# Performance work log

Hardware: AMD Instinct MI355X
Metric: run time of the kernel (lower is better)

## Reference

```python
import jax, jax.numpy as jnp
import numpy as np

SCALE = 100.0
ACTIVE_EPS = 1e-6


def setup_inputs() -> dict:
    key = jax.random.key(0)
    kq, kk, kv = jax.random.split(key, 3)
    B, K, D = 64, 1024, 512
    return {
        "query": jax.random.normal(kq, (B, D), dtype=jnp.float32),
        "keys": jax.random.normal(kk, (K, D), dtype=jnp.float32),
        "values": jax.random.normal(kv, (K, D), dtype=jnp.float32),
    }


def _scores(query, keys):
    # Fused, batched version of the per-key PureFFN score layers.
    # Layer k has W_up = diag(S * key[k] * d^-0.5) on active dims (|key|>1e-6),
    # b_gate = 1 on active dims, W_down[0] = 1/S on active dims. The extra
    # hidden unit (row `dim`) has zero W_down weight and never contributes.
    # PureFFN: out = W_down @ (h * sigmoid(h + b_gate)), h = W_up @ x.
    D = query.shape[-1]
    scale = D ** -0.5
    active = (jnp.abs(keys) > ACTIVE_EPS).astype(query.dtype)      # [K, D]
    u = (SCALE * scale) * query[:, None, :] * keys[None, :, :]     # [B, K, D]
    g = u * jax.nn.sigmoid(u + active[None, :, :])                 # silu with b_gate=1 on active dims
    return (1.0 / SCALE) * jnp.einsum('bkd,kd->bk', g, active)    # [B, K]


def reference(query, keys, values):
    scores = _scores(query, keys)            # [B, K]
    winner_idx = jnp.argmax(scores, axis=-1)  # [B] int
    out_values = values[winner_idx]           # [B, D] winner-take-all gather
    return out_values, winner_idx
```

## Files before the change

kernel.cpp:

```cpp
#include <hip/hip_runtime.h>
#include <stdint.h>

#define NB 64
#define NK 1024
#define ND 512
#define ROWS 2
#define CHUNKS 64
#define KEYS_PER_BLOCK (NK / CHUNKS)
#define WAVES_PER_BLOCK 4
#define KEYS_PER_WAVE (KEYS_PER_BLOCK / WAVES_PER_BLOCK)

typedef float v2f __attribute__((ext_vector_type(2)));

#if __has_builtin(__builtin_amdgcn_exp2f)
#define EXP2F(x) __builtin_amdgcn_exp2f(x)
#else
#define EXP2F(x) exp2f(x)
#endif
#if __has_builtin(__builtin_amdgcn_rcpf)
#define RCPF(x) __builtin_amdgcn_rcpf(x)
#else
#define RCPF(x) (1.0f / (x))
#endif

__device__ __forceinline__ void silu2_acc(v2f qc, v2f kv, v2f& acc) {
    const float NL2E = -1.4426950408889634f;
    v2f u = qc * kv;
    v2f y = u * NL2E + NL2E;
    v2f e;
    e.x = EXP2F(y.x);
    e.y = EXP2F(y.y);
    v2f f = e + 1.0f;
    float r = RCPF(f.x * f.y);
    v2f sg;
    sg.x = r * f.y;
    sg.y = r * f.x;
    acc += u * sg;
}

__device__ __forceinline__ unsigned long long pack_win(float s, int k) {
    uint32_t bits = __float_as_uint(s);
    uint32_t so = (bits & 0x80000000u) ? ~bits : (bits | 0x80000000u);
    return ((unsigned long long)so << 32) | (unsigned long long)(uint32_t)(NK - 1 - k);
}

__global__ __launch_bounds__(256, 8) void sia_scores(const float* __restrict__ q,
                                                     const float* __restrict__ keys,
                                                     unsigned long long* __restrict__ ws) {
    const int bidx = blockIdx.x;
    const int bg    = bidx >> 6;
    const int chunk = bidx & (CHUNKS - 1);
    const int tid = threadIdx.x;
    const int wave = tid >> 6;
    const int lane = tid & 63;

    const float C = 100.0f * 0.04419417382415922f;

    v2f qv[ROWS][4];
    #pragma unroll
    for (int r = 0; r < ROWS; ++r) {
        const v2f* q2 = reinterpret_cast<const v2f*>(q + (bg * ROWS + r) * ND + lane * 8);
        #pragma unroll
        for (int j = 0; j < 4; ++j)
            qv[r][j] = q2[j] * C;
    }

    const int k0 = chunk * KEYS_PER_BLOCK + wave * KEYS_PER_WAVE;

    v2f acc[ROWS][KEYS_PER_WAVE];
    #pragma unroll
    for (int r = 0; r < ROWS; ++r)
        #pragma unroll
        for (int i = 0; i < KEYS_PER_WAVE; ++i)
            acc[r][i] = (v2f)0.0f;

    #pragma unroll
    for (int i = 0; i < KEYS_PER_WAVE; ++i) {
        const float4* k4 = reinterpret_cast<const float4*>(keys + (k0 + i) * ND + lane * 8);
        float4 ka = k4[0];
        float4 kb = k4[1];
        v2f kv[4];
        kv[0] = (v2f){ka.x, ka.y};
        kv[1] = (v2f){ka.z, ka.w};
        kv[2] = (v2f){kb.x, kb.y};
        kv[3] = (v2f){kb.z, kb.w};
        #pragma unroll
        for (int r = 0; r < ROWS; ++r)
            #pragma unroll
            for (int j = 0; j < 4; ++j)
                silu2_acc(qv[r][j], kv[j], acc[r][i]);
    }

    float sc[ROWS][KEYS_PER_WAVE];
    #pragma unroll
    for (int r = 0; r < ROWS; ++r)
        #pragma unroll
        for (int i = 0; i < KEYS_PER_WAVE; ++i)
            sc[r][i] = acc[r][i].x + acc[r][i].y;

    #pragma unroll
    for (int off = 32; off > 0; off >>= 1) {
        #pragma unroll
        for (int r = 0; r < ROWS; ++r)
            #pragma unroll
            for (int i = 0; i < KEYS_PER_WAVE; ++i)
                sc[r][i] += __shfl_xor(sc[r][i], off, 64);
    }

    __shared__ unsigned long long win[WAVES_PER_BLOCK][ROWS];
    if (lane == 0) {
        #pragma unroll
        for (int r = 0; r < ROWS; ++r) {
            float best_s = sc[r][0];
            int best_j = 0;
            #pragma unroll
            for (int i = 1; i < KEYS_PER_WAVE; ++i)
                if (sc[r][i] > best_s) { best_s = sc[r][i]; best_j = i; }
            win[wave][r] = pack_win(best_s, k0 + best_j);
        }
    }
    __syncthreads();

    if (tid < ROWS) {
        const int r = tid;
        unsigned long long p = win[0][r];
        #pragma unroll
        for (int w = 1; w < WAVES_PER_BLOCK; ++w)
            if (win[w][r] > p) p = win[w][r];
        ws[(bg * ROWS + r) * CHUNKS + chunk] = p;
    }
}

__global__ __launch_bounds__(128) void sia_final(const unsigned long long* __restrict__ ws,
                                                 const float* __restrict__ values,
                                                 float* __restrict__ out) {
    const int b = blockIdx.x;
    const int tid = threadIdx.x;
    const int lane = tid & 63;

    unsigned long long p = ws[b * CHUNKS + lane];
    #pragma unroll
    for (int off = 32; off > 0; off >>= 1) {
        unsigned long long o = __shfl_xor(p, off, 64);
        if (o > p) p = o;
    }
    const int k = NK - 1 - (int)((uint32_t)p & 0x3FFu);

    const float4* v4 = reinterpret_cast<const float4*>(values + (size_t)k * ND);
    float4* o4 = reinterpret_cast<float4*>(out + b * ND);
    o4[tid] = v4[tid];

    if (tid == 0)
        out[NB * ND + b] = (float)k;
}

extern "C" void kernel_launch(void* const* d_in, const int* in_sizes, int n_in,
                              void* d_out, int out_size, void* d_ws, size_t ws_size,
                              hipStream_t stream) {
    const float* q      = (const float*)d_in[0];
    const float* keys   = (const float*)d_in[1];
    const float* values = (const float*)d_in[2];
    float* out = (float*)d_out;
    unsigned long long* ws = (unsigned long long*)d_ws;

    sia_scores<<<dim3((NB / ROWS) * CHUNKS), dim3(256), 0, stream>>>(q, keys, ws);
    sia_final<<<dim3(NB), dim3(128), 0, stream>>>(ws, values, out);
}
```

Measured before the change: 16.44 us.

## Use transpose-style butterfly reduction and halve key chunks per batch group

Replaces the per-key full-wave shuffle reductions with a recursive halving exchange that reduces all row/key combos together, then finds the argmax across lanes with packed-key shuffles. The number of key chunks is halved so each wave processes 8 keys, and the occupancy hint is lowered to 4 blocks. This aims to cut cross-lane shuffle traffic and the serial lane-0 argmax. The trade-off is fewer blocks and more registers per thread.

Result: slower. 22.13 us (+34.6%).

```diff
diff --git a/kernel.cpp b/kernel.cpp
--- a/kernel.cpp
+++ b/kernel.cpp
@@ -5,10 +5,11 @@
 #define NK 1024
 #define ND 512
 #define ROWS 2
-#define CHUNKS 64
-#define KEYS_PER_BLOCK (NK / CHUNKS)
-#define WAVES_PER_BLOCK 4
-#define KEYS_PER_WAVE (KEYS_PER_BLOCK / WAVES_PER_BLOCK)
+#define CHUNKS 32
+#define KPB (NK / CHUNKS)
+#define WPB 4
+#define KPW (KPB / WPB)
+#define NCOMBO (ROWS * KPW)
 
 typedef float v2f __attribute__((ext_vector_type(2)));
 
@@ -44,11 +45,11 @@
     return ((unsigned long long)so << 32) | (unsigned long long)(uint32_t)(NK - 1 - k);
 }
 
-__global__ __launch_bounds__(256, 8) void sia_scores(const float* __restrict__ q,
+__global__ __launch_bounds__(256, 4) void sia_scores(const float* __restrict__ q,
                                                      const float* __restrict__ keys,
                                                      unsigned long long* __restrict__ ws) {
     const int bidx = blockIdx.x;
-    const int bg    = bidx >> 6;
+    const int bg    = bidx >> 5;
     const int chunk = bidx & (CHUNKS - 1);
     const int tid = threadIdx.x;
     const int wave = tid >> 6;
@@ -65,17 +66,17 @@
             qv[r][j] = q2[j] * C;
     }
 
-    const int k0 = chunk * KEYS_PER_BLOCK + wave * KEYS_PER_WAVE;
+    const int k0 = chunk * KPB + wave * KPW;
 
-    v2f acc[ROWS][KEYS_PER_WAVE];
+    v2f acc[ROWS][KPW];
     #pragma unroll
     for (int r = 0; r < ROWS; ++r)
         #pragma unroll
-        for (int i = 0; i < KEYS_PER_WAVE; ++i)
+        for (int i = 0; i < KPW; ++i)
             acc[r][i] = (v2f)0.0f;
 
     #pragma unroll
-    for (int i = 0; i < KEYS_PER_WAVE; ++i) {
+    for (int i = 0; i < KPW; ++i) {
         const float4* k4 = reinterpret_cast<const float4*>(keys + (k0 + i) * ND + lane * 8);
         float4 ka = k4[0];
         float4 kb = k4[1];
@@ -91,43 +92,48 @@
                 silu2_acc(qv[r][j], kv[j], acc[r][i]);
     }
 
-    float sc[ROWS][KEYS_PER_WAVE];
+    float val[NCOMBO];
     #pragma unroll
     for (int r = 0; r < ROWS; ++r)
         #pragma unroll
-        for (int i = 0; i < KEYS_PER_WAVE; ++i)
-            sc[r][i] = acc[r][i].x + acc[r][i].y;
+        for (int i = 0; i < KPW; ++i)
+            val[r * KPW + i] = acc[r][i].x + acc[r][i].y;
 
     #pragma unroll
-    for (int off = 32; off > 0; off >>= 1) {
+    for (int b = 32, h = NCOMBO / 2; b >= 4; b >>= 1, h >>= 1) {
         #pragma unroll
-        for (int r = 0; r < ROWS; ++r)
-            #pragma unroll
-            for (int i = 0; i < KEYS_PER_WAVE; ++i)
-                sc[r][i] += __shfl_xor(sc[r][i], off, 64);
+        for (int i = 0; i < h; ++i) {
+            float send = (lane & b) ? val[i] : val[i + h];
+            float recv = __shfl_xor(send, b, 64);
+            float keep = (lane & b) ? val[i + h] : val[i];
+            val[i] = keep + recv;
+        }
+    }
+    float v = val[0];
+    v += __shfl_xor(v, 2, 64);
+    v += __shfl_xor(v, 1, 64);
+
+    const int j = (lane >> 2) & 7;
+    unsigned long long p = pack_win(v, k0 + j);
+
+    #pragma unroll
+    for (int o = 16; o >= 1; o >>= 1) {
+        unsigned long long t = __shfl_xor(p, o, 64);
+        if (t > p) p = t;
     }
 
-    __shared__ unsigned long long win[WAVES_PER_BLOCK][ROWS];
-    if (lane == 0) {
-        #pragma unroll
-        for (int r = 0; r < ROWS; ++r) {
-            float best_s = sc[r][0];
-            int best_j = 0;
-            #pragma unroll
-            for (int i = 1; i < KEYS_PER_WAVE; ++i)
-                if (sc[r][i] > best_s) { best_s = sc[r][i]; best_j = i; }
-            win[wave][r] = pack_win(best_s, k0 + best_j);
-        }
-    }
+    __shared__ unsigned long long win[WPB][ROWS];
+    if (lane == 0)  win[wave][0] = p;
+    if (lane == 32) win[wave][1] = p;
     __syncthreads();
 
     if (tid < ROWS) {
         const int r = tid;
-        unsigned long long p = win[0][r];
+        unsigned long long w = win[0][r];
         #pragma unroll
-        for (int w = 1; w < WAVES_PER_BLOCK; ++w)
-            if (win[w][r] > p) p = win[w][r];
-        ws[(bg * ROWS + r) * CHUNKS + chunk] = p;
+        for (int ww = 1; ww < WPB; ++ww)
+            if (win[ww][r] > w) w = win[ww][r];
+        ws[(bg * ROWS + r) * CHUNKS + chunk] = w;
     }
 }
 
@@ -138,11 +144,11 @@
     const int tid = threadIdx.x;
     const int lane = tid & 63;
 
-    unsigned long long p = ws[b * CHUNKS + lane];
+    unsigned long long p = ws[b * CHUNKS + (lane & 31)];
     #pragma unroll
-    for (int off = 32; off > 0; off >>= 1) {
-        unsigned long long o = __shfl_xor(p, off, 64);
-        if (o > p) p = o;
+    for (int o = 16; o >= 1; o >>= 1) {
+        unsigned long long t = __shfl_xor(p, o, 64);
+        if (t > p) p = t;
     }
     const int k = NK - 1 - (int)((uint32_t)p & 0x3FFu);
 
```

## Split each wave into four 16-lane key groups with strided float4 loads

Applied to the files above, without the earlier changes.

Each wave now handles four keys at once, with 16 lanes per key. Lanes load interleaved float4 segments, so each load is fully coalesced across 16 lanes and each lane keeps only two accumulators instead of eight per row. The reduction becomes a 16-lane shuffle sum followed by a packed argmax shuffle across groups, replacing the full 64-lane reduction and the serial scan on lane 0. The query register footprint grows to 8 float4 per row, and launch bounds drop to 4 blocks per SM to allow for the extra registers.

New measurement: 16.25 us. No clear change (-1.1%).

```diff
diff --git a/kernel.cpp b/kernel.cpp
--- a/kernel.cpp
+++ b/kernel.cpp
@@ -6,9 +6,8 @@
 #define ND 512
 #define ROWS 2
 #define CHUNKS 64
-#define KEYS_PER_BLOCK (NK / CHUNKS)
-#define WAVES_PER_BLOCK 4
-#define KEYS_PER_WAVE (KEYS_PER_BLOCK / WAVES_PER_BLOCK)
+#define KPB (NK / CHUNKS)
+#define WPB 4
 
 typedef float v2f __attribute__((ext_vector_type(2)));
 
@@ -44,7 +43,7 @@
     return ((unsigned long long)so << 32) | (unsigned long long)(uint32_t)(NK - 1 - k);
 }
 
-__global__ __launch_bounds__(256, 8) void sia_scores(const float* __restrict__ q,
+__global__ __launch_bounds__(256, 4) void sia_scores(const float* __restrict__ q,
                                                      const float* __restrict__ keys,
                                                      unsigned long long* __restrict__ ws) {
     const int bidx = blockIdx.x;
@@ -53,81 +52,72 @@
     const int tid = threadIdx.x;
     const int wave = tid >> 6;
     const int lane = tid & 63;
+    const int s = lane & 15;
 
     const float C = 100.0f * 0.04419417382415922f;
 
-    v2f qv[ROWS][4];
+    const int k0 = chunk * KPB + wave * 4;
+    const int kg = k0 + ((lane >> 4) & 3);
+
+    float4 qv[ROWS][8];
     #pragma unroll
     for (int r = 0; r < ROWS; ++r) {
-        const v2f* q2 = reinterpret_cast<const v2f*>(q + (bg * ROWS + r) * ND + lane * 8);
+        const float4* q4 = reinterpret_cast<const float4*>(q + (bg * ROWS + r) * ND) + s;
         #pragma unroll
-        for (int j = 0; j < 4; ++j)
-            qv[r][j] = q2[j] * C;
+        for (int j = 0; j < 8; ++j) {
+            float4 t = q4[j * 16];
+            t.x *= C; t.y *= C; t.z *= C; t.w *= C;
+            qv[r][j] = t;
+        }
     }
 
-    const int k0 = chunk * KEYS_PER_BLOCK + wave * KEYS_PER_WAVE;
-
-    v2f acc[ROWS][KEYS_PER_WAVE];
+    const float4* kp = reinterpret_cast<const float4*>(keys + (size_t)kg * ND) + s;
+    v2f acc0[ROWS] = {(v2f)0.0f, (v2f)0.0f};
+    v2f acc1[ROWS] = {(v2f)0.0f, (v2f)0.0f};
     #pragma unroll
-    for (int r = 0; r < ROWS; ++r)
+    for (int j = 0; j < 8; ++j) {
+        float4 kv = kp[j * 16];
+        v2f klo = (v2f){kv.x, kv.y};
+        v2f khi = (v2f){kv.z, kv.w};
         #pragma unroll
-        for (int i = 0; i < KEYS_PER_WAVE; ++i)
-            acc[r][i] = (v2f)0.0f;
-
-    #pragma unroll
-    for (int i = 0; i < KEYS_PER_WAVE; ++i) {
-        const float4* k4 = reinterpret_cast<const float4*>(keys + (k0 + i) * ND + lane * 8);
-        float4 ka = k4[0];
-        float4 kb = k4[1];
-        v2f kv[4];
-        kv[0] = (v2f){ka.x, ka.y};
-        kv[1] = (v2f){ka.z, ka.w};
-        kv[2] = (v2f){kb.x, kb.y};
-        kv[3] = (v2f){kb.z, kb.w};
-        #pragma unroll
-        for (int r = 0; r < ROWS; ++r)
-            #pragma unroll
-            for (int j = 0; j < 4; ++j)
-                silu2_acc(qv[r][j], kv[j], acc[r][i]);
+        for (int r = 0; r < ROWS; ++r) {
+            silu2_acc((v2f){qv[r][j].x, qv[r][j].y}, klo, acc0[r]);
+            silu2_acc((v2f){qv[r][j].z, qv[r][j].w}, khi, acc1[r]);
+        }
     }
 
-    float sc[ROWS][KEYS_PER_WAVE];
+    v2f sc;
+    sc.x = (acc0[0].x + acc0[0].y) + (acc1[0].x + acc1[0].y);
+    sc.y = (acc0[1].x + acc0[1].y) + (acc1[1].x + acc1[1].y);
     #pragma unroll
-    for (int r = 0; r < ROWS; ++r)
-        #pragma unroll
-        for (int i = 0; i < KEYS_PER_WAVE; ++i)
-            sc[r][i] = acc[r][i].x + acc[r][i].y;
-
-    #pragma unroll
-    for (int off = 32; off > 0; off >>= 1) {
-        #pragma unroll
-        for (int r = 0; r < ROWS; ++r)
-            #pragma unroll
-            for (int i = 0; i < KEYS_PER_WAVE; ++i)
-                sc[r][i] += __shfl_xor(sc[r][i], off, 64);
+    for (int off = 8; off >= 1; off >>= 1) {
+        v2f o;
+        o.x = __shfl_xor(sc.x, off, 64);
+        o.y = __shfl_xor(sc.y, off, 64);
+        sc += o;
     }
 
-    __shared__ unsigned long long win[WAVES_PER_BLOCK][ROWS];
-    if (lane == 0) {
-        #pragma unroll
-        for (int r = 0; r < ROWS; ++r) {
-            float best_s = sc[r][0];
-            int best_j = 0;
-            #pragma unroll
-            for (int i = 1; i < KEYS_PER_WAVE; ++i)
-                if (sc[r][i] > best_s) { best_s = sc[r][i]; best_j = i; }
-            win[wave][r] = pack_win(best_s, k0 + best_j);
-        }
+    unsigned long long p0 = pack_win(sc.x, kg);
+    unsigned long long p1 = pack_win(sc.y, kg);
+    #pragma unroll
+    for (int off = 16; off <= 32; off <<= 1) {
+        unsigned long long t0 = __shfl_xor(p0, off, 64);
+        unsigned long long t1 = __shfl_xor(p1, off, 64);
+        if (t0 > p0) p0 = t0;
+        if (t1 > p1) p1 = t1;
     }
+
+    __shared__ unsigned long long win[WPB][ROWS];
+    if (lane == 0) { win[wave][0] = p0; win[wave][1] = p1; }
     __syncthreads();
 
     if (tid < ROWS) {
         const int r = tid;
-        unsigned long long p = win[0][r];
+        unsigned long long w = win[0][r];
         #pragma unroll
-        for (int w = 1; w < WAVES_PER_BLOCK; ++w)
-            if (win[w][r] > p) p = win[w][r];
-        ws[(bg * ROWS + r) * CHUNKS + chunk] = p;
+        for (int ww = 1; ww < WPB; ++ww)
+            if (win[ww][r] > w) w = win[ww][r];
+        ws[(bg * ROWS + r) * CHUNKS + chunk] = w;
     }
 }
 
```
